# Optimization experiments

Hardware: AMD Instinct MI355X
Metric: run time of the kernel (lower is better)

The kernel has to match this reference:

```python
import jax, jax.numpy as jnp
import numpy as np

B, S, HID = 2, 1024, 4096
H, KV, D = 32, 8, 128
EPS = 1e-6
ROPE_THETA = 1000000.0


def _make_freqs_cis(seq_len, head_dim, theta):
    inv_freq = 1.0 / (theta ** (jnp.arange(0, head_dim, 2, dtype=jnp.float32) / head_dim))
    ang = jnp.arange(seq_len, dtype=jnp.float32)[:, None] * inv_freq[None, :]  # [S, D/2]
    emb = jnp.concatenate([ang, ang], axis=-1)                                 # [S, D]
    cos, sin = jnp.cos(emb), jnp.sin(emb)
    return jnp.stack([cos, sin, -sin], axis=0)                                 # [3, S, D]


def setup_inputs() -> dict:
    key = jax.random.key(0)
    ks = jax.random.split(key, 8)
    scale = 0.02
    return {
        "hidden_states": jax.random.normal(ks[0], (B, S, HID), dtype=jnp.float32),
        "freqs_cis": _make_freqs_cis(S, D, ROPE_THETA),
        "Wq": jax.random.normal(ks[1], (H * D, HID), dtype=jnp.float32) * scale,
        "Wk": jax.random.normal(ks[2], (KV * D, HID), dtype=jnp.float32) * scale,
        "Wv": jax.random.normal(ks[3], (KV * D, HID), dtype=jnp.float32) * scale,
        "Wo": jax.random.normal(ks[4], (HID, H * D), dtype=jnp.float32) * scale,
        "q_norm_w": jnp.ones((D,), jnp.float32) + jax.random.normal(ks[5], (D,), jnp.float32) * scale,
        "k_norm_w": jnp.ones((D,), jnp.float32) + jax.random.normal(ks[6], (D,), jnp.float32) * scale,
    }


def _rmsnorm(x, w):
    # per-head RMSNorm over last dim (rms_norm_add=False -> plain weight multiply)
    return x * jax.lax.rsqrt(jnp.mean(x * x, axis=-1, keepdims=True) + EPS) * w


def _rope(x, cos, sin, nsin):
    # matches apply_rope: e = x*cos; e[:half] += x[half:]*nsin; e[half:] += x[:half]*sin
    half = x.shape[-1] // 2
    e = x * cos
    lo = e[..., :half] + x[..., half:] * nsin[..., :half]
    hi = e[..., half:] + x[..., :half] * sin[..., half:]
    return jnp.concatenate([lo, hi], axis=-1)


def reference(hidden_states, freqs_cis, Wq, Wk, Wv, Wo, q_norm_w, k_norm_w):
    b, s, _ = hidden_states.shape
    # QKV projections (no bias)
    q = jnp.einsum("bsh,oh->bso", hidden_states, Wq).reshape(b, s, H, D).transpose(0, 2, 1, 3)
    k = jnp.einsum("bsh,oh->bso", hidden_states, Wk).reshape(b, s, KV, D).transpose(0, 2, 1, 3)
    v = jnp.einsum("bsh,oh->bso", hidden_states, Wv).reshape(b, s, KV, D).transpose(0, 2, 1, 3)
    # per-head RMSNorm (Qwen3 'gemma3' q/k norms)
    q = _rmsnorm(q, q_norm_w)
    k = _rmsnorm(k, k_norm_w)
    # RoPE
    cos, sin, nsin = freqs_cis[0], freqs_cis[1], freqs_cis[2]  # [S, D] each, broadcast over (b, heads)
    q = _rope(q, cos, sin, nsin)
    k = _rope(k, cos, sin, nsin)
    # GQA: repeat kv heads to match query heads (repeat_interleave dim=1)
    rep = H // KV
    k = jnp.repeat(k, rep, axis=1)
    v = jnp.repeat(v, rep, axis=1)
    # SDPA (no mask, past_key_value=None path)
    scale = D ** -0.5
    attn = jax.nn.softmax(jnp.einsum("bhqd,bhkd->bhqk", q, k) * scale, axis=-1)
    out = jnp.einsum("bhqk,bhkd->bhqd", attn, v)
    out = out.transpose(0, 2, 1, 3).reshape(b, s, H * D)
    return jnp.einsum("bsi,hi->bsh", out, Wo)
```

## Files before the change

### kernel.cpp

```cpp
#include <hip/hip_runtime.h>


typedef __attribute__((ext_vector_type(8))) short s8v;
typedef __attribute__((ext_vector_type(4))) float f4v;
typedef __attribute__((ext_vector_type(8))) unsigned short u8v;
typedef __attribute__((ext_vector_type(4))) float float4v;
typedef __attribute__((ext_vector_type(2))) float float2v;
typedef unsigned short us;

#define SB() __builtin_amdgcn_sched_barrier(0)

__device__ __forceinline__ void BARRIER() {
  asm volatile("" ::: "memory");
  __builtin_amdgcn_s_barrier();
  asm volatile("" ::: "memory");
}

__device__ __forceinline__ us f2b(float f) {
  unsigned u = __builtin_bit_cast(unsigned, f);
  u += 0x7fffu + ((u >> 16) & 1u);
  return (us)(u >> 16);
}
__device__ __forceinline__ float b2f(us h) {
  return __builtin_bit_cast(float, (unsigned)h << 16);
}

__device__ __forceinline__ void gload16(const void* g, void* l) {
  __builtin_amdgcn_global_load_lds(
      (const __attribute__((address_space(1))) unsigned int*)g,
      (__attribute__((address_space(3))) unsigned int*)l, 16, 0, 0);
}

__global__ __launch_bounds__(256) void cvt_all_k(const float* __restrict__ h,
                                                 const float* __restrict__ wq,
                                                 const float* __restrict__ wk,
                                                 const float* __restrict__ wv,
                                                 us* __restrict__ dst) {
  long blk = blockIdx.x;
  const float* src;
  long off;
  if (blk < 4096)        { src = h;  off = 0; }
  else if (blk < 12288)  { src = wq; off = 4096; }
  else if (blk < 14336)  { src = wk; off = 12288; }
  else                   { src = wv; off = 14336; }
  long i = (blk - off) * 2048 + (long)threadIdx.x * 8;
  long o = blk * 2048 + (long)threadIdx.x * 8;
  float4v a = *(const float4v*)(src + i);
  float4v b = *(const float4v*)(src + i + 4);
  u8v v;
  v[0] = f2b(a[0]); v[1] = f2b(a[1]); v[2] = f2b(a[2]); v[3] = f2b(a[3]);
  v[4] = f2b(b[0]); v[5] = f2b(b[1]); v[6] = f2b(b[2]); v[7] = f2b(b[3]);
  *(u8v*)(dst + o) = v;
}

template <int AH, bool F32OUT, bool CVTTAIL>
__global__ __launch_bounds__(512, 2) void gemm8p(const us* __restrict__ A,
                                                 const us* __restrict__ W,
                                                 void* __restrict__ Cv,
                                                 int K, int nkt, int ldc,
                                                 int cm, int cn, int ncn,
                                                 int nGemm,
                                                 const float* __restrict__ csrc,
                                                 us* __restrict__ cdst) {
  if constexpr (CVTTAIL) {
    if ((int)blockIdx.x >= nGemm) {
      long c = (long)((int)blockIdx.x - nGemm) * 512 + threadIdx.x;
      for (; c < 2097152; c += 64 * 512) {
        long i = c * 8;
        float4v x = *(const float4v*)(csrc + i);
        float4v y = *(const float4v*)(csrc + i + 4);
        u8v v;
        v[0] = f2b(x[0]); v[1] = f2b(x[1]); v[2] = f2b(x[2]); v[3] = f2b(x[3]);
        v[4] = f2b(y[0]); v[5] = f2b(y[1]); v[6] = f2b(y[2]); v[7] = f2b(y[3]);
        *(u8v*)(cdst + i) = v;
      }
      return;
    }
  }

  constexpr int FR = AH / 32;
  constexpr int LA = AH / 64;
  constexpr int VM = 2 * LA + 2;

  __shared__ __align__(16) us Ah[2][2][AH * 64];
  __shared__ __align__(16) us Bh[2][2][128 * 64];
  const int tid = threadIdx.x, lane = tid & 63, w = tid >> 6;
  const int wr = w >> 2, wc = w & 3;
  const int lr = lane & 15, lg = lane >> 4;

  const int xcd = (int)blockIdx.x & 7;
  const int i2 = (int)blockIdx.x >> 3;
  const int im = i2 % cm, itn = i2 / cm;
  const long m0 = (long)((xcd / ncn) * cm + im) * (2 * AH);
  const long n0 = (long)((xcd % ncn) * cn + itn) * 256;

  const int rA0 = tid >> 3;
  const int sc0 = ((tid & 7) ^ (rA0 & 7)) << 3;

#define STGH(dst, src, LOADS)                                           \
  do {                                                                  \
    const us* _s = (src);                                               \
    us* _d = (dst);                                                     \
    _Pragma("unroll") for (int l = 0; l < (LOADS); ++l)                 \
      gload16(_s + (long)(rA0 + l * 64) * K + sc0, _d + (l * 512 + tid) * 8); \
  } while (0)

  const us* Asrc = A + m0 * K;
  const us* Bsrc = W + n0 * K;
  const long hKA = (long)AH * K;
  const long hKB = (long)128 * K;

  const int ra = wr * (AH / 2) + lr, rb = wc * 32 + lr;
  const int offA0 = ra * 64 + ((lg ^ (ra & 7)) << 3);
  const int offA1 = ra * 64 + (((4 + lg) ^ (ra & 7)) << 3);
  const int offB0 = rb * 64 + ((lg ^ (rb & 7)) << 3);
  const int offB1 = rb * 64 + (((4 + lg) ^ (rb & 7)) << 3);

  f4v acc[2 * FR][4];
#pragma unroll
  for (int i = 0; i < 2 * FR; ++i)
#pragma unroll
    for (int j = 0; j < 4; ++j) acc[i][j] = (f4v){0.f, 0.f, 0.f, 0.f};

  const int nk = nkt;

  STGH(Ah[0][0], Asrc, LA);
  STGH(Bh[0][0], Bsrc, 2);
  STGH(Bh[0][1], Bsrc + hKB, 2);
  STGH(Ah[0][1], Asrc + hKA, LA);
  STGH(Ah[1][0], Asrc + 64, LA);
  STGH(Bh[1][1], Bsrc + hKB + 64, 2);
  STGH(Ah[1][1], Asrc + hKA + 64, LA);
  asm volatile("s_waitcnt vmcnt(%0)" :: "i"(VM) : "memory");
  BARRIER();

  s8v a[FR][2], b0[2][2], b1[2][2];

#define RD_A(H)                                                         \
  _Pragma("unroll") for (int f = 0; f < FR; ++f) {                      \
    a[f][0] = *(const s8v*)(&Ah[d][H][offA0 + f * 1024]);               \
    a[f][1] = *(const s8v*)(&Ah[d][H][offA1 + f * 1024]);               \
  }
#define RD_B(BB, H)                                                     \
  _Pragma("unroll") for (int g = 0; g < 2; ++g) {                       \
    BB[g][0] = *(const s8v*)(&Bh[d][H][offB0 + g * 1024]);              \
    BB[g][1] = *(const s8v*)(&Bh[d][H][offB1 + g * 1024]);              \
  }
#define QUAD(QM, QN, BB)                                                \
  __builtin_amdgcn_s_setprio(1);                                        \
  _Pragma("unroll") for (int f = 0; f < FR; ++f)                        \
  _Pragma("unroll") for (int g = 0; g < 2; ++g) {                       \
    f4v t = acc[QM * FR + f][QN * 2 + g];                               \
    t = __builtin_amdgcn_mfma_f32_16x16x32_bf16(a[f][0], BB[g][0], t, 0, 0, 0); \
    t = __builtin_amdgcn_mfma_f32_16x16x32_bf16(a[f][1], BB[g][1], t, 0, 0, 0); \
    acc[QM * FR + f][QN * 2 + g] = t;                                   \
  }                                                                     \
  __builtin_amdgcn_s_setprio(0);
#define PREMFMA()                                                       \
  BARRIER();                                                            \
  asm volatile("s_waitcnt lgkmcnt(0)" ::: "memory");                    \
  SB();

  for (int kt = 0; kt < nk; ++kt) {
    const int d = kt & 1;
    const long kb2 = (long)(kt + 2) * 64;
    const bool p1 = (kt + 1 < nk), p2 = (kt + 2 < nk);

    RD_A(0)
    RD_B(b0, 0)
    if (p1) STGH(Bh[d ^ 1][0], Bsrc + (long)(kt + 1) * 64, 2);
    PREMFMA()
    QUAD(0, 0, b0)
    BARRIER();

    RD_B(b1, 1)
    if (p2) STGH(Ah[d][0], Asrc + kb2, LA);
    PREMFMA()
    QUAD(0, 1, b1)
    BARRIER();

    RD_A(1)
    if (p2) STGH(Bh[d][1], Bsrc + hKB + kb2, 2);
    PREMFMA()
    QUAD(1, 1, b1)
    BARRIER();

    if (p2) STGH(Ah[d][1], Asrc + hKA + kb2, LA);
    PREMFMA()
    QUAD(1, 0, b0)
    if (p2) asm volatile("s_waitcnt vmcnt(%0)" :: "i"(VM) : "memory");
    else    asm volatile("s_waitcnt vmcnt(0)" ::: "memory");
    BARRIER();
  }

#pragma unroll
  for (int qm = 0; qm < 2; ++qm)
#pragma unroll
    for (int f = 0; f < FR; ++f) {
      long row = m0 + qm * AH + wr * (AH / 2) + f * 16 + lg * 4;
#pragma unroll
      for (int qn = 0; qn < 2; ++qn)
#pragma unroll
        for (int g = 0; g < 2; ++g) {
          long col = n0 + qn * 128 + wc * 32 + g * 16 + lr;
          f4v v = acc[qm * FR + f][qn * 2 + g];
          if constexpr (F32OUT) {
            float* C = (float*)Cv;
#pragma unroll
            for (int r = 0; r < 4; ++r) C[(row + r) * ldc + col] = v[r];
          } else {
            us* C = (us*)Cv;
#pragma unroll
            for (int r = 0; r < 4; ++r) C[(row + r) * ldc + col] = f2b(v[r]);
          }
        }
    }
#undef STGH
#undef RD_A
#undef RD_B
#undef QUAD
#undef PREMFMA
}

__global__ __launch_bounds__(256, 2) void gemm2p128(const us* __restrict__ A,
                                                    const us* __restrict__ W,
                                                    float* __restrict__ C) {
  constexpr int K = 4096, nk = 64, ldc = 4096;
  __shared__ __align__(16) us Ab[2][128 * 64];
  __shared__ __align__(16) us Bb[2][128 * 64];
  const int tid = threadIdx.x, lane = tid & 63, w = tid >> 6;
  const int wm = w & 1, wn = w >> 1;
  const int lr = lane & 15, lg = lane >> 4;

  const int xcd = (int)blockIdx.x & 7;
  const int i2 = (int)blockIdx.x >> 3;
  const long m0 = (long)(i2 & 15) * 128;
  const long n0 = (long)(xcd * 4 + (i2 >> 4)) * 128;

  const int rA0 = tid >> 3;
  const int sc0 = ((tid & 7) ^ (rA0 & 7)) << 3;

  const us* Asrc = A + m0 * K;
  const us* Bsrc = W + n0 * K;

#define STG1(Sb, buf, src)                                               \
  do {                                                                   \
    const us* _s = (src);                                                \
    _Pragma("unroll") for (int l = 0; l < 4; ++l)                        \
      gload16(_s + (long)(rA0 + l * 32) * K + sc0,                       \
              &Sb[buf][(l * 256 + tid) * 8]);                            \
  } while (0)

  const int ra = wm * 64 + lr;
  const int rb = wn * 64 + lr;
  const int offA0 = ra * 64 + ((lg ^ (ra & 7)) << 3);
  const int offA1 = ra * 64 + (((4 + lg) ^ (ra & 7)) << 3);
  const int offB0 = rb * 64 + ((lg ^ (rb & 7)) << 3);
  const int offB1 = rb * 64 + (((4 + lg) ^ (rb & 7)) << 3);

  f4v acc[4][4];
#pragma unroll
  for (int f = 0; f < 4; ++f)
#pragma unroll
    for (int g = 0; g < 4; ++g) acc[f][g] = (f4v){0.f, 0.f, 0.f, 0.f};

  STG1(Ab, 0, Asrc);
  STG1(Bb, 0, Bsrc);
  STG1(Ab, 1, Asrc + 64);
  asm volatile("s_waitcnt vmcnt(4)" ::: "memory");
  BARRIER();

  for (int kt = 0; kt < nk; ++kt) {
    const int d = kt & 1;
    const bool p1 = (kt + 1 < nk), p2 = (kt + 2 < nk);

    s8v a[4][2], b[4][2];
#pragma unroll
    for (int f = 0; f < 4; ++f) {
      a[f][0] = *(const s8v*)(&Ab[d][offA0 + f * 1024]);
      a[f][1] = *(const s8v*)(&Ab[d][offA1 + f * 1024]);
    }
#pragma unroll
    for (int g = 0; g < 4; ++g) {
      b[g][0] = *(const s8v*)(&Bb[d][offB0 + g * 1024]);
      b[g][1] = *(const s8v*)(&Bb[d][offB1 + g * 1024]);
    }
    if (p1) STG1(Bb, d ^ 1, Bsrc + (long)(kt + 1) * 64);
    asm volatile("s_waitcnt lgkmcnt(0)" ::: "memory");
    BARRIER();
    if (p2) STG1(Ab, d, Asrc + (long)(kt + 2) * 64);

    __builtin_amdgcn_s_setprio(1);
#pragma unroll
    for (int f = 0; f < 4; ++f)
#pragma unroll
      for (int g = 0; g < 4; ++g) {
        f4v t = acc[f][g];
        t = __builtin_amdgcn_mfma_f32_16x16x32_bf16(a[f][0], b[g][0], t, 0, 0, 0);
        t = __builtin_amdgcn_mfma_f32_16x16x32_bf16(a[f][1], b[g][1], t, 0, 0, 0);
        acc[f][g] = t;
      }
    __builtin_amdgcn_s_setprio(0);

    if (p2) asm volatile("s_waitcnt vmcnt(4)" ::: "memory");
    else    asm volatile("s_waitcnt vmcnt(0)" ::: "memory");
    BARRIER();
  }

#pragma unroll
  for (int f = 0; f < 4; ++f) {
    long row = m0 + wm * 64 + f * 16 + lg * 4;
#pragma unroll
    for (int g = 0; g < 4; ++g) {
      long col = n0 + wn * 64 + g * 16 + lr;
      f4v v = acc[f][g];
#pragma unroll
      for (int r = 0; r < 4; ++r) C[(row + r) * ldc + col] = v[r];
    }
  }
#undef STG1
}

__global__ __launch_bounds__(256) void rms_rope_k(us* __restrict__ qkv,
                                                  const float* __restrict__ fc,
                                                  const float* __restrict__ kw) {
  int idx = blockIdx.x * 4 + (threadIdx.x >> 6);
  int lane = threadIdx.x & 63;
  int head = idx & 7;
  int row = idx >> 3;
  int s = row & 1023;
  us* p = qkv + (long)row * 6144 + 4096 + head * 128;

  unsigned v = ((const unsigned*)p)[lane];
  float x0 = b2f((us)(v & 0xffff)), x1 = b2f((us)(v >> 16));
  float ss = x0 * x0 + x1 * x1;
#pragma unroll
  for (int off = 32; off; off >>= 1) ss += __shfl_xor(ss, off);
  float r = rsqrtf(ss * (1.0f / 128.0f) + 1e-6f);
  float2v wv = ((const float2v*)kw)[lane];
  float y0 = x0 * r * wv[0], y1 = x1 * r * wv[1];
  float py0 = __shfl(y0, lane ^ 32);
  float py1 = __shfl(y1, lane ^ 32);
  float2v cv = ((const float2v*)(fc + (long)s * 128))[lane];
  const float* sbase = (lane < 32) ? (fc + 2 * 1024 * 128) : (fc + 1024 * 128);
  float2v sv = ((const float2v*)(sbase + (long)s * 128))[lane];
  float e0 = y0 * cv[0] + py0 * sv[0];
  float e1 = y1 * cv[1] + py1 * sv[1];
  ((unsigned*)p)[lane] = (unsigned)f2b(e0) | ((unsigned)f2b(e1) << 16);
}

__global__ __launch_bounds__(256) void attn_k(const us* __restrict__ qkv,
                                              us* __restrict__ ao,
                                              const float* __restrict__ fc,
                                              const float* __restrict__ qw) {
  __shared__ us Kt[64 * 128];
  __shared__ us Vt[128 * 72];
  __shared__ us Pl[4 * 1024];

  const int bid = blockIdx.x;
  const int qt = bid & 15;
  const int h = (bid >> 4) & 31;
  const int b = bid >> 9;
  const int kvh = h >> 2;
  const int tid = threadIdx.x, lane = tid & 63, w = tid >> 6;
  const int lr = lane & 15, lg = lane >> 4;

  const int srow = qt * 64 + w * 16 + lr;
  const us* Qb = qkv + (long)(b * 1024 + srow) * 6144 + h * 128;
  s8v qr[4];
#pragma unroll
  for (int ks = 0; ks < 4; ++ks) qr[ks] = *(const s8v*)(Qb + ks * 32 + lg * 8);

  float ssq = 0.f;
#pragma unroll
  for (int ks = 0; ks < 4; ++ks)
#pragma unroll
    for (int j = 0; j < 8; ++j) {
      float x = b2f((us)qr[ks][j]);
      ssq += x * x;
    }
  ssq += __shfl_xor(ssq, 16);
  ssq += __shfl_xor(ssq, 32);
  const float rr = rsqrtf(ssq * (1.0f / 128.0f) + 1e-6f);

  const float* cosp = fc + (long)srow * 128;
  const float* sinp = fc + 1024 * 128 + (long)srow * 128;
  s8v qf[4];
#pragma unroll
  for (int ks = 0; ks < 4; ++ks) {
    const int d0 = ks * 32 + lg * 8;
    const int dp = d0 ^ 64;
    const float sgn = (ks < 2) ? -1.f : 1.f;
#pragma unroll
    for (int j = 0; j < 8; ++j) {
      float y  = b2f((us)qr[ks][j])     * rr * qw[d0 + j];
      float yp = b2f((us)qr[ks ^ 2][j]) * rr * qw[dp + j];
      float e = y * cosp[d0 + j] + yp * sgn * sinp[d0 + j];
      qf[ks][j] = (short)f2b(e);
    }
  }

  f4v o[8];
#pragma unroll
  for (int n = 0; n < 8; ++n) o[n] = (f4v){0.f, 0.f, 0.f, 0.f};
  float m[4], l[4];
#pragma unroll
  for (int r = 0; r < 4; ++r) { m[r] = -1e30f; l[r] = 0.f; }

  const float SL = 0.08838834764831845f * 1.4426950408889634f;
  const long krow = (long)b * 1024 * 6144 + 4096 + kvh * 128;
  const long vrow = (long)b * 1024 * 6144 + 5120 + kvh * 128;

  for (int kt = 0; kt < 16; ++kt) {
    __syncthreads();
#pragma unroll
    for (int t = 0; t < 4; ++t) {
      int c = t * 256 + tid;
      int row = c >> 4;
      int sc = (c & 15) ^ (row & 7);
      gload16(qkv + krow + (long)(kt * 64 + row) * 6144 + sc * 8, &Kt[c * 8]);
    }
#pragma unroll
    for (int t = 0; t < 2; ++t) {
      int c = t * 256 + tid;
      int kp = c & 31;
      int d0 = (c >> 5) * 8;
      const us* vsrc = qkv + vrow + (long)(kt * 64) * 6144 + d0;
      s8v va = *(const s8v*)(vsrc + (long)(2 * kp) * 6144);
      s8v vb = *(const s8v*)(vsrc + (long)(2 * kp + 1) * 6144);
#pragma unroll
      for (int i = 0; i < 8; ++i) {
        unsigned pk = (unsigned)(us)va[i] | ((unsigned)(us)vb[i] << 16);
        *(unsigned*)&Vt[(d0 + i) * 72 + 2 * kp] = pk;
      }
    }
    __syncthreads();

    f4v sacc[4];
#pragma unroll
    for (int j = 0; j < 4; ++j) sacc[j] = (f4v){0.f, 0.f, 0.f, 0.f};
    __builtin_amdgcn_s_setprio(1);
#pragma unroll
    for (int ks = 0; ks < 4; ++ks) {
#pragma unroll
      for (int j = 0; j < 4; ++j) {
        int key = j * 16 + lr;
        s8v kf = *(const s8v*)&Kt[key * 128 + (((ks * 64 + lg * 16) ^ ((key & 7) << 4)) >> 1)];
        sacc[j] = __builtin_amdgcn_mfma_f32_16x16x32_bf16(qf[ks], kf, sacc[j], 0, 0, 0);
      }
    }
    __builtin_amdgcn_s_setprio(0);

    float sm[4];
#pragma unroll
    for (int r = 0; r < 4; ++r)
      sm[r] = fmaxf(fmaxf(sacc[0][r], sacc[1][r]), fmaxf(sacc[2][r], sacc[3][r]));
#pragma unroll
    for (int off = 1; off < 16; off <<= 1)
#pragma unroll
      for (int r = 0; r < 4; ++r) sm[r] = fmaxf(sm[r], __shfl_xor(sm[r], off));
    float alpha[4];
#pragma unroll
    for (int r = 0; r < 4; ++r) {
      float nm = fmaxf(m[r], sm[r] * SL);
      alpha[r] = exp2f(m[r] - nm);
      m[r] = nm;
      l[r] *= alpha[r];
    }
#pragma unroll
    for (int n = 0; n < 8; ++n)
#pragma unroll
      for (int r = 0; r < 4; ++r) o[n][r] *= alpha[r];

    us* pw = Pl + w * 1024;
#pragma unroll
    for (int j = 0; j < 4; ++j)
#pragma unroll
      for (int r = 0; r < 4; ++r) {
        float p = exp2f(sacc[j][r] * SL - m[r]);
        l[r] += p;
        int prow = lg * 4 + r, pcol = j * 16 + lr;
        pw[(prow * 128 + ((pcol * 2) ^ ((prow & 7) << 4))) >> 1] = f2b(p);
      }

    __builtin_amdgcn_s_setprio(1);
#pragma unroll
    for (int ks = 0; ks < 2; ++ks) {
      int bo = ks * 64 + lg * 16;
      s8v pf = *(const s8v*)&Pl[w * 1024 + ((lr * 128 + (bo ^ ((lr & 7) << 4))) >> 1)];
#pragma unroll
      for (int n = 0; n < 8; ++n) {
        s8v vf = *(const s8v*)&Vt[(n * 16 + lr) * 72 + ks * 32 + lg * 8];
        o[n] = __builtin_amdgcn_mfma_f32_16x16x32_bf16(pf, vf, o[n], 0, 0, 0);
      }
    }
    __builtin_amdgcn_s_setprio(0);
  }

#pragma unroll
  for (int off = 1; off < 16; off <<= 1)
#pragma unroll
    for (int r = 0; r < 4; ++r) l[r] += __shfl_xor(l[r], off);
  float inv[4];
#pragma unroll
  for (int r = 0; r < 4; ++r) inv[r] = 1.f / l[r];
  const long ob = (long)(b * 1024 + qt * 64 + w * 16) * 4096 + h * 128;
#pragma unroll
  for (int n = 0; n < 8; ++n)
#pragma unroll
    for (int r = 0; r < 4; ++r)
      ao[ob + (long)(lg * 4 + r) * 4096 + n * 16 + lr] = f2b(o[n][r] * inv[r]);
}

extern "C" void kernel_launch(void* const* d_in, const int* in_sizes, int n_in,
                              void* d_out, int out_size, void* d_ws, size_t ws_size,
                              hipStream_t stream) {
  const float* hidden = (const float*)d_in[0];
  const float* fc     = (const float*)d_in[1];
  const float* Wq     = (const float*)d_in[2];
  const float* Wk     = (const float*)d_in[3];
  const float* Wv     = (const float*)d_in[4];
  const float* Wo     = (const float*)d_in[5];
  const float* qw     = (const float*)d_in[6];
  const float* kw     = (const float*)d_in[7];

  us* hb  = (us*)d_ws;
  us* wb  = hb + (long)2048 * 4096;
  us* wbo = wb + (long)6144 * 4096;
  us* qkv = wbo + (long)4096 * 4096;
  us* ao  = qkv + (long)2048 * 6144;

  cvt_all_k<<<16384, 256, 0, stream>>>(hidden, Wq, Wk, Wv, hb);

  gemm8p<128, false, true><<<256, 512, 0, stream>>>(
      hb, wb, qkv, 4096, 64, 6144, 4, 6, 4, 192, Wo, wbo);

  rms_rope_k<<<4096, 256, 0, stream>>>(qkv, fc, kw);

  attn_k<<<1024, 256, 0, stream>>>(qkv, ao, fc, qw);

  gemm2p128<<<512, 256, 0, stream>>>(ao, wbo, (float*)d_out);
}
```

Baseline: 316.1 us.

## Switch GEMM kernels from 16x16x32 to 32x32x16 bf16 MFMA tiles

Both GEMM kernels (the fused QKV projection and the output projection) now use the 32x32x16 bf16 MFMA instruction instead of 16x16x32. Fragment loads, accumulator layout and epilogue row/column mapping are reworked to match the 32x32 output layout. The larger MFMA needs fewer LDS fragment reads per FLOP and fewer instructions, which is meant to improve compute throughput. In exchange it uses larger accumulator vectors, adds register pressure, and requires a different swizzled LDS read pattern that could create bank conflicts.

```diff
diff --git a/kernel.cpp b/kernel.cpp
--- a/kernel.cpp
+++ b/kernel.cpp
@@ -3,6 +3,7 @@
 
 typedef __attribute__((ext_vector_type(8))) short s8v;
 typedef __attribute__((ext_vector_type(4))) float f4v;
+typedef __attribute__((ext_vector_type(16))) float f16v;
 typedef __attribute__((ext_vector_type(8))) unsigned short u8v;
 typedef __attribute__((ext_vector_type(4))) float float4v;
 typedef __attribute__((ext_vector_type(2))) float float2v;
@@ -78,7 +79,6 @@
     }
   }
 
-  constexpr int FR = AH / 32;
   constexpr int LA = AH / 64;
   constexpr int VM = 2 * LA + 2;
 
@@ -86,7 +86,8 @@
   __shared__ __align__(16) us Bh[2][2][128 * 64];
   const int tid = threadIdx.x, lane = tid & 63, w = tid >> 6;
   const int wr = w >> 2, wc = w & 3;
-  const int lr = lane & 15, lg = lane >> 4;
+  const int lg = lane >> 4;
+  const int l31 = lane & 31, lh = lane >> 5, xa = lane & 7;
 
   const int xcd = (int)blockIdx.x & 7;
   const int i2 = (int)blockIdx.x >> 3;
@@ -110,17 +111,18 @@
   const long hKA = (long)AH * K;
   const long hKB = (long)128 * K;
 
-  const int ra = wr * (AH / 2) + lr, rb = wc * 32 + lr;
-  const int offA0 = ra * 64 + ((lg ^ (ra & 7)) << 3);
-  const int offA1 = ra * 64 + (((4 + lg) ^ (ra & 7)) << 3);
-  const int offB0 = rb * 64 + ((lg ^ (rb & 7)) << 3);
-  const int offB1 = rb * 64 + (((4 + lg) ^ (rb & 7)) << 3);
-
-  f4v acc[2 * FR][4];
-#pragma unroll
-  for (int i = 0; i < 2 * FR; ++i)
-#pragma unroll
-    for (int j = 0; j < 4; ++j) acc[i][j] = (f4v){0.f, 0.f, 0.f, 0.f};
+  const int rowA0 = wr * (AH / 2) + l31;
+  const int rowB0 = wc * 32 + l31;
+
+  f16v acc[2][2][LA];
+#pragma unroll
+  for (int qm = 0; qm < 2; ++qm)
+#pragma unroll
+    for (int qn = 0; qn < 2; ++qn)
+#pragma unroll
+      for (int f = 0; f < LA; ++f)
+#pragma unroll
+        for (int r = 0; r < 16; ++r) acc[qm][qn][f][r] = 0.f;
 
   const int nk = nkt;
 
@@ -134,26 +136,24 @@
   asm volatile("s_waitcnt vmcnt(%0)" :: "i"(VM) : "memory");
   BARRIER();
 
-  s8v a[FR][2], b0[2][2], b1[2][2];
+  s8v a[LA][4], b0[4], b1[4];
 
 #define RD_A(H)                                                         \
-  _Pragma("unroll") for (int f = 0; f < FR; ++f) {                      \
-    a[f][0] = *(const s8v*)(&Ah[d][H][offA0 + f * 1024]);               \
-    a[f][1] = *(const s8v*)(&Ah[d][H][offA1 + f * 1024]);               \
-  }
+  _Pragma("unroll") for (int f = 0; f < LA; ++f)                        \
+  _Pragma("unroll") for (int s = 0; s < 4; ++s)                         \
+    a[f][s] = *(const s8v*)(&Ah[d][H][(rowA0 + f * 32) * 64 +           \
+                                      (((2 * s + lh) ^ xa) << 3)]);
 #define RD_B(BB, H)                                                     \
-  _Pragma("unroll") for (int g = 0; g < 2; ++g) {                       \
-    BB[g][0] = *(const s8v*)(&Bh[d][H][offB0 + g * 1024]);              \
-    BB[g][1] = *(const s8v*)(&Bh[d][H][offB1 + g * 1024]);              \
-  }
+  _Pragma("unroll") for (int s = 0; s < 4; ++s)                         \
+    BB[s] = *(const s8v*)(&Bh[d][H][rowB0 * 64 +                        \
+                                    (((2 * s + lh) ^ xa) << 3)]);
 #define QUAD(QM, QN, BB)                                                \
   __builtin_amdgcn_s_setprio(1);                                        \
-  _Pragma("unroll") for (int f = 0; f < FR; ++f)                        \
-  _Pragma("unroll") for (int g = 0; g < 2; ++g) {                       \
-    f4v t = acc[QM * FR + f][QN * 2 + g];                               \
-    t = __builtin_amdgcn_mfma_f32_16x16x32_bf16(a[f][0], BB[g][0], t, 0, 0, 0); \
-    t = __builtin_amdgcn_mfma_f32_16x16x32_bf16(a[f][1], BB[g][1], t, 0, 0, 0); \
-    acc[QM * FR + f][QN * 2 + g] = t;                                   \
+  _Pragma("unroll") for (int f = 0; f < LA; ++f) {                      \
+    f16v t = acc[QM][QN][f];                                            \
+    _Pragma("unroll") for (int s = 0; s < 4; ++s)                       \
+      t = __builtin_amdgcn_mfma_f32_32x32x16_bf16(a[f][s], BB[s], t, 0, 0, 0); \
+    acc[QM][QN][f] = t;                                                 \
   }                                                                     \
   __builtin_amdgcn_s_setprio(0);
 #define PREMFMA()                                                       \
@@ -196,24 +196,19 @@
 #pragma unroll
   for (int qm = 0; qm < 2; ++qm)
 #pragma unroll
-    for (int f = 0; f < FR; ++f) {
-      long row = m0 + qm * AH + wr * (AH / 2) + f * 16 + lg * 4;
-#pragma unroll
-      for (int qn = 0; qn < 2; ++qn)
-#pragma unroll
-        for (int g = 0; g < 2; ++g) {
-          long col = n0 + qn * 128 + wc * 32 + g * 16 + lr;
-          f4v v = acc[qm * FR + f][qn * 2 + g];
-          if constexpr (F32OUT) {
-            float* C = (float*)Cv;
-#pragma unroll
-            for (int r = 0; r < 4; ++r) C[(row + r) * ldc + col] = v[r];
-          } else {
-            us* C = (us*)Cv;
-#pragma unroll
-            for (int r = 0; r < 4; ++r) C[(row + r) * ldc + col] = f2b(v[r]);
-          }
+    for (int f = 0; f < LA; ++f) {
+      long RB = m0 + qm * AH + wr * (AH / 2) + f * 32 + 4 * lh;
+#pragma unroll
+      for (int qn = 0; qn < 2; ++qn) {
+        long CB = n0 + qn * 128 + wc * 32 + l31;
+        f16v v = acc[qm][qn][f];
+#pragma unroll
+        for (int r = 0; r < 16; ++r) {
+          long row = RB + (r & 3) + 8 * (r >> 2);
+          if constexpr (F32OUT) ((float*)Cv)[row * ldc + CB] = v[r];
+          else                  ((us*)Cv)[row * ldc + CB] = f2b(v[r]);
         }
+      }
     }
 #undef STGH
 #undef RD_A
@@ -230,7 +225,7 @@
   __shared__ __align__(16) us Bb[2][128 * 64];
   const int tid = threadIdx.x, lane = tid & 63, w = tid >> 6;
   const int wm = w & 1, wn = w >> 1;
-  const int lr = lane & 15, lg = lane >> 4;
+  const int l31 = lane & 31, lh = lane >> 5, xa = lane & 7;
 
   const int xcd = (int)blockIdx.x & 7;
   const int i2 = (int)blockIdx.x >> 3;
@@ -251,18 +246,16 @@
               &Sb[buf][(l * 256 + tid) * 8]);                            \
   } while (0)
 
-  const int ra = wm * 64 + lr;
-  const int rb = wn * 64 + lr;
-  const int offA0 = ra * 64 + ((lg ^ (ra & 7)) << 3);
-  const int offA1 = ra * 64 + (((4 + lg) ^ (ra & 7)) << 3);
-  const int offB0 = rb * 64 + ((lg ^ (rb & 7)) << 3);
-  const int offB1 = rb * 64 + (((4 + lg) ^ (rb & 7)) << 3);
-
-  f4v acc[4][4];
-#pragma unroll
-  for (int f = 0; f < 4; ++f)
-#pragma unroll
-    for (int g = 0; g < 4; ++g) acc[f][g] = (f4v){0.f, 0.f, 0.f, 0.f};
+  const int rowA0 = wm * 64 + l31;
+  const int rowB0 = wn * 64 + l31;
+
+  f16v acc[2][2];
+#pragma unroll
+  for (int f = 0; f < 2; ++f)
+#pragma unroll
+    for (int g = 0; g < 2; ++g)
+#pragma unroll
+      for (int r = 0; r < 16; ++r) acc[f][g][r] = 0.f;
 
   STG1(Ab, 0, Asrc);
   STG1(Bb, 0, Bsrc);
@@ -274,17 +267,19 @@
     const int d = kt & 1;
     const bool p1 = (kt + 1 < nk), p2 = (kt + 2 < nk);
 
-    s8v a[4][2], b[4][2];
-#pragma unroll
-    for (int f = 0; f < 4; ++f) {
-      a[f][0] = *(const s8v*)(&Ab[d][offA0 + f * 1024]);
-      a[f][1] = *(const s8v*)(&Ab[d][offA1 + f * 1024]);
-    }
-#pragma unroll
-    for (int g = 0; g < 4; ++g) {
-      b[g][0] = *(const s8v*)(&Bb[d][offB0 + g * 1024]);
-      b[g][1] = *(const s8v*)(&Bb[d][offB1 + g * 1024]);
-    }
+    s8v a[2][4], b[2][4];
+#pragma unroll
+    for (int f = 0; f < 2; ++f)
+#pragma unroll
+      for (int s = 0; s < 4; ++s)
+        a[f][s] = *(const s8v*)(&Ab[d][(rowA0 + f * 32) * 64 +
+                                       (((2 * s + lh) ^ xa) << 3)]);
+#pragma unroll
+    for (int g = 0; g < 2; ++g)
+#pragma unroll
+      for (int s = 0; s < 4; ++s)
+        b[g][s] = *(const s8v*)(&Bb[d][(rowB0 + g * 32) * 64 +
+                                       (((2 * s + lh) ^ xa) << 3)]);
     if (p1) STG1(Bb, d ^ 1, Bsrc + (long)(kt + 1) * 64);
     asm volatile("s_waitcnt lgkmcnt(0)" ::: "memory");
     BARRIER();
@@ -292,12 +287,13 @@
 
     __builtin_amdgcn_s_setprio(1);
 #pragma unroll
-    for (int f = 0; f < 4; ++f)
-#pragma unroll
-      for (int g = 0; g < 4; ++g) {
-        f4v t = acc[f][g];
-        t = __builtin_amdgcn_mfma_f32_16x16x32_bf16(a[f][0], b[g][0], t, 0, 0, 0);
-        t = __builtin_amdgcn_mfma_f32_16x16x32_bf16(a[f][1], b[g][1], t, 0, 0, 0);
+    for (int f = 0; f < 2; ++f)
+#pragma unroll
+      for (int g = 0; g < 2; ++g) {
+        f16v t = acc[f][g];
+#pragma unroll
+        for (int s = 0; s < 4; ++s)
+          t = __builtin_amdgcn_mfma_f32_32x32x16_bf16(a[f][s], b[g][s], t, 0, 0, 0);
         acc[f][g] = t;
       }
     __builtin_amdgcn_s_setprio(0);
@@ -308,14 +304,17 @@
   }
 
 #pragma unroll
-  for (int f = 0; f < 4; ++f) {
-    long row = m0 + wm * 64 + f * 16 + lg * 4;
-#pragma unroll
-    for (int g = 0; g < 4; ++g) {
-      long col = n0 + wn * 64 + g * 16 + lr;
-      f4v v = acc[f][g];
-#pragma unroll
-      for (int r = 0; r < 4; ++r) C[(row + r) * ldc + col] = v[r];
+  for (int f = 0; f < 2; ++f) {
+    long RB = m0 + wm * 64 + f * 32 + 4 * lh;
+#pragma unroll
+    for (int g = 0; g < 2; ++g) {
+      long CB = n0 + wn * 64 + g * 32 + l31;
+      f16v v = acc[f][g];
+#pragma unroll
+      for (int r = 0; r < 16; ++r) {
+        long row = RB + (r & 3) + 8 * (r >> 2);
+        C[row * ldc + CB] = v[r];
+      }
     }
   }
 #undef STG1
```

Result: slower. 339.4 us (+7.4%).
